# Performance work log

Hardware: AMD Instinct MI355X
Metric: run time of the kernel (lower is better)

The kernel has to match this reference:

```python
import jax, jax.numpy as jnp
import numpy as np


def setup_inputs() -> dict:
    key = jax.random.key(0)
    k_x, k_w1, k_b1, k_w2, k_b2 = jax.random.split(key, 5)
    N, D, H = 4_000_000, 10, 16
    x = jax.random.normal(k_x, (N, D), dtype=jnp.float32)
    # torch.nn.Linear default init: U(-1/sqrt(fan_in), 1/sqrt(fan_in))
    lim1 = 1.0 / np.sqrt(D)
    W1 = jax.random.uniform(k_w1, (H, D), minval=-lim1, maxval=lim1, dtype=jnp.float32)
    b1 = jax.random.uniform(k_b1, (H,), minval=-lim1, maxval=lim1, dtype=jnp.float32)
    lim2 = 1.0 / np.sqrt(H)
    W2 = jax.random.uniform(k_w2, (1, H), minval=-lim2, maxval=lim2, dtype=jnp.float32)
    b2 = jax.random.uniform(k_b2, (1,), minval=-lim2, maxval=lim2, dtype=jnp.float32)
    return {"x": x, "W1": W1, "b1": b1, "W2": W2, "b2": b2}


def reference(x, W1, b1, W2, b2):
    # Gram matrix: (10, 10)
    y = x.T @ x
    # symmetric eigendecomposition; w: eigenvectors (10, 10), ascending eigenvalues
    v, w = jnp.linalg.eigh(y)
    h = jax.nn.relu(w @ W1.T + b1)          # (10, 16)
    o = h @ W2.T + b2                        # (10, 1)
    return 0.5 * (jax.nn.sigmoid(o) + 1.0)
```

## Files before the change

### kernel.cpp

```cpp
#include <hip/hip_runtime.h>
#include <math.h>

#pragma clang fp contract(off)

#define NACC 55
#define KC_DEFAULT 384
#define FOLD_LDS 12288

__device__ __forceinline__ void group_load(const float4* __restrict__ xv,
                                           long g, float4* buf) {
#pragma unroll
  for (int t = 0; t < 20; ++t) buf[t] = xv[g * 20 + t];
}

__device__ __forceinline__ void pair_fma_one(const float4 q0, const float4 q1,
                                             const float4 q2, const float4 q3,
                                             const float4 q4, float* acc) {
  float a[10] = {q0.x, q0.y, q0.z, q0.w, q1.x, q1.y, q1.z, q1.w, q2.x, q2.y};
  float b[10] = {q2.z, q2.w, q3.x, q3.y, q3.z, q3.w, q4.x, q4.y, q4.z, q4.w};
  int e = 0;
#pragma unroll
  for (int i = 0; i < 10; ++i)
#pragma unroll
    for (int j = 0; j <= i; ++j) {
      acc[e] = __builtin_fmaf(a[i], a[j], acc[e]);
      acc[e] = __builtin_fmaf(b[i], b[j], acc[e]);
      ++e;
    }
}

__device__ __forceinline__ void group_fma(const float4* buf, float* acc) {
#pragma unroll
  for (int pp = 0; pp < 4; ++pp)
    pair_fma_one(buf[pp * 5 + 0], buf[pp * 5 + 1], buf[pp * 5 + 2],
                 buf[pp * 5 + 3], buf[pp * 5 + 4], acc);
}

__global__ __launch_bounds__(64, 1) void gram32_kernel(
    const float* __restrict__ x, float* __restrict__ partial,
    int nrows, int kc, int nchunks, int prow) {
  int c = blockIdx.x * 64 + threadIdx.x;
  if (c >= nchunks) return;
  long k0 = (long)c * kc;
  long rem = (long)nrows - k0;
  int klen = rem < kc ? (int)rem : kc;

  float acc[NACC];
#pragma unroll
  for (int e = 0; e < NACC; ++e) acc[e] = 0.0f;

  const float4* __restrict__ xv = (const float4*)(x + k0 * 10);
  int npair = klen >> 1;
  int ngrp = npair >> 2;

  float4 bufA[20], bufB[20];

  int g = 0;
  if (ngrp > 0) group_load(xv, 0, bufA);
  while (g < ngrp) {
    if (g + 1 < ngrp) group_load(xv, g + 1, bufB);
    group_fma(bufA, acc);
    ++g;
    if (g >= ngrp) break;
    if (g + 1 < ngrp) group_load(xv, g + 1, bufA);
    group_fma(bufB, acc);
    ++g;
  }
  for (int p = ngrp * 4; p < npair; ++p) {
    float4 v0 = xv[(long)p * 5 + 0];
    float4 v1 = xv[(long)p * 5 + 1];
    float4 v2 = xv[(long)p * 5 + 2];
    float4 v3 = xv[(long)p * 5 + 3];
    float4 v4 = xv[(long)p * 5 + 4];
    pair_fma_one(v0, v1, v2, v3, v4, acc);
  }
  if (klen & 1) {
    const float* row = x + (k0 + klen - 1) * 10;
    float a[10];
#pragma unroll
    for (int i = 0; i < 10; ++i) a[i] = row[i];
    int e = 0;
#pragma unroll
    for (int i = 0; i < 10; ++i)
#pragma unroll
      for (int j = 0; j <= i; ++j) {
        acc[e] = __builtin_fmaf(a[i], a[j], acc[e]);
        ++e;
      }
  }
#pragma unroll
  for (int e = 0; e < NACC; ++e)
    partial[(long)e * prow + c] = acc[e];
}

__global__ __launch_bounds__(256) void fold32_kernel(
    const float* __restrict__ partial, float* __restrict__ G, int nchunks,
    int prow) {
  __shared__ float buf[FOLD_LDS];
  int e = blockIdx.x;
  const float* p = partial + (long)e * prow;

  if (nchunks <= FOLD_LDS) {
    int n4 = nchunks >> 2;
    const float4* p4 = (const float4*)p;
    float4* b4 = (float4*)buf;
    for (int i = threadIdx.x; i < n4; i += 256) b4[i] = p4[i];
    for (int i = (n4 << 2) + threadIdx.x; i < nchunks; i += 256)
      buf[i] = p[i];
    __syncthreads();
    if (threadIdx.x == 0) {
      float s = buf[0];
      int c = 1;
      for (; c + 16 <= nchunks; c += 16) {
        float v[16];
#pragma unroll
        for (int t = 0; t < 16; ++t) v[t] = buf[c + t];
#pragma unroll
        for (int t = 0; t < 16; ++t) s = s + v[t];
      }
      for (; c < nchunks; ++c) s = s + buf[c];
      G[e] = s;
    }
  } else {
    if (threadIdx.x == 0) {
      float s = p[0];
      for (int c = 1; c < nchunks; ++c) s = s + p[c];
      G[e] = s;
    }
  }
}

__device__ __forceinline__ float rdlane(float v, int l) {
  return __int_as_float(__builtin_amdgcn_readlane(__float_as_int(v), l));
}
__device__ __forceinline__ float s_sign(float a, float b) {
  return copysignf(fabsf(a), b);
}
__device__ __forceinline__ float slapy2(float x, float y) {
  float xa = fabsf(x), ya = fabsf(y);
  float w = fmaxf(xa, ya), z = fminf(xa, ya);
  if (z == 0.0f) return w;
  float t = z / w;
  return w * sqrtf(1.0f + t * t);
}
__device__ __forceinline__ void slartg(float f, float g, float* c, float* s,
                                       float* r) {
  float d = sqrtf(f * f + g * g);
  float cg = fabsf(f) / d;
  float rg = s_sign(d, f);
  float sg = g / rg;
  bool g0 = (g == 0.0f);
  bool f0 = (f == 0.0f);
  *c = g0 ? 1.0f : (f0 ? 0.0f : cg);
  *s = g0 ? 0.0f : (f0 ? s_sign(1.0f, g) : sg);
  *r = g0 ? f : (f0 ? fabsf(g) : rg);
}
__device__ void slaev2(float a, float b, float c, float* rt1, float* rt2,
                       float* cs1, float* sn1) {
  float sm = a + c, df = a - c;
  float adf = fabsf(df);
  float tb = b + b;
  float ab = fabsf(tb);
  float acmx, acmn;
  if (fabsf(a) > fabsf(c)) { acmx = a; acmn = c; } else { acmx = c; acmn = a; }
  float rt;
  if (adf > ab) { float t = ab / adf; rt = adf * sqrtf(1.0f + t * t); }
  else if (adf < ab) { float t = adf / ab; rt = ab * sqrtf(1.0f + t * t); }
  else rt = ab * sqrtf(2.0f);
  int sgn1;
  if (sm < 0.0f) {
    *rt1 = 0.5f * (sm - rt); sgn1 = -1;
    *rt2 = (acmx / *rt1) * acmn - (b / *rt1) * b;
  } else if (sm > 0.0f) {
    *rt1 = 0.5f * (sm + rt); sgn1 = 1;
    *rt2 = (acmx / *rt1) * acmn - (b / *rt1) * b;
  } else {
    *rt1 = 0.5f * rt; *rt2 = -0.5f * rt; sgn1 = 1;
  }
  int sgn2;
  float cs;
  if (df >= 0.0f) { cs = df + rt; sgn2 = 1; } else { cs = df - rt; sgn2 = -1; }
  float acs = fabsf(cs);
  if (acs > ab) {
    float ct = -tb / cs;
    *sn1 = 1.0f / sqrtf(1.0f + ct * ct);
    *cs1 = ct * (*sn1);
  } else {
    if (ab == 0.0f) { *cs1 = 1.0f; *sn1 = 0.0f; }
    else {
      float tn = -cs / tb;
      *cs1 = 1.0f / sqrtf(1.0f + tn * tn);
      *sn1 = tn * (*cs1);
    }
  }
  if (sgn1 == sgn2) { float tn = *cs1; *cs1 = -(*sn1); *sn1 = tn; }
}

#define GETD(i) ((i)==0?d0:(i)==1?d1:(i)==2?d2:(i)==3?d3:(i)==4?d4:(i)==5?d5:(i)==6?d6:(i)==7?d7:(i)==8?d8:d9)
#define PUTD(i,v) do{int _i=(i);float _x=(v);d0=(_i==0)?_x:d0;d1=(_i==1)?_x:d1;d2=(_i==2)?_x:d2;d3=(_i==3)?_x:d3;d4=(_i==4)?_x:d4;d5=(_i==5)?_x:d5;d6=(_i==6)?_x:d6;d7=(_i==7)?_x:d7;d8=(_i==8)?_x:d8;d9=(_i==9)?_x:d9;}while(0)
#define GETZ(i) ((i)==0?z0:(i)==1?z1:(i)==2?z2:(i)==3?z3:(i)==4?z4:(i)==5?z5:(i)==6?z6:(i)==7?z7:(i)==8?z8:z9)
#define PUTZ(i,v) do{int _i=(i);float _x=(v);z0=(_i==0)?_x:z0;z1=(_i==1)?_x:z1;z2=(_i==2)?_x:z2;z3=(_i==3)?_x:z3;z4=(_i==4)?_x:z4;z5=(_i==5)?_x:z5;z6=(_i==6)?_x:z6;z7=(_i==7)?_x:z7;z8=(_i==8)?_x:z8;z9=(_i==9)?_x:z9;}while(0)

__global__ __launch_bounds__(64, 1) void solve_kernel(
    const float* __restrict__ Gp, const float* __restrict__ W1,
    const float* __restrict__ b1, const float* __restrict__ W2,
    const float* __restrict__ b2, float* __restrict__ out) {
  __shared__ float zbuf[10 * 11];
  __shared__ float abuf[10 * 11];
  const int lane = threadIdx.x;
  const int myrow = lane < 10 ? lane : 9;

  float row[10];
#pragma unroll
  for (int c = 0; c < 10; ++c) {
    int rr = myrow >= c ? myrow : c;
    int cc = myrow >= c ? c : myrow;
    row[c] = Gp[rr * (rr + 1) / 2 + cc];
  }

  float dv = 0.0f, ev = 0.0f;
  float tau[9];

#pragma unroll
  for (int i = 0; i < 9; ++i) {
    float v[10];
    {
      float myci = row[i];
#pragma unroll
      for (int k = 0; k < 10; ++k) v[k] = rdlane(myci, k);
    }
    float alpha = v[i + 1];
    float xn2 = 0.0f;
#pragma unroll
    for (int k = i + 2; k < 10; ++k) xn2 = xn2 + v[k] * v[k];
    float xnorm = sqrtf(xn2);
    float taui;
    if (xnorm == 0.0f) {
      taui = 0.0f;
      ev = (lane == i) ? alpha : ev;
    } else {
      float beta = -s_sign(slapy2(alpha, xnorm), alpha);
      taui = (beta - alpha) / beta;
      float sc = 1.0f / (alpha - beta);
#pragma unroll
      for (int k = i + 2; k < 10; ++k) v[k] = v[k] * sc;
      if (lane >= i + 2 && lane < 10) row[i] = row[i] * sc;
      if (lane == i) {
#pragma unroll
        for (int c = i + 2; c < 10; ++c) row[c] = row[c] * sc;
      }
      if (lane == i + 1) row[i] = beta;
      if (lane == i) row[i + 1] = beta;
      ev = (lane == i) ? beta : ev;
    }
    if (taui != 0.0f) {
      v[i + 1] = 1.0f;
      float vme = (lane == i + 1)
                      ? 1.0f
                      : ((lane >= i + 2 && lane < 10) ? row[i] : 0.0f);
      float s = 0.0f;
#pragma unroll
      for (int c2 = i + 1; c2 < 10; ++c2) s = s + row[c2] * v[c2];
      float pvr = taui * s;
      float pva[10];
#pragma unroll
      for (int k = 0; k < 10; ++k) pva[k] = rdlane(pvr, k);
      float dot = 0.0f;
#pragma unroll
      for (int k = i + 1; k < 10; ++k) dot = dot + pva[k] * v[k];
      float alpha2 = -0.5f * taui * dot;
      pvr = pvr + alpha2 * vme;
#pragma unroll
      for (int k = 0; k < 10; ++k) pva[k] = pva[k] + alpha2 * v[k];
      if (lane >= i + 1 && lane < 10) {
#pragma unroll
        for (int c2 = i + 1; c2 < 10; ++c2)
          row[c2] = row[c2] - (vme * pva[c2] + pvr * v[c2]);
      }
    }
    tau[i] = taui;
    {
      float t = rdlane(row[i], i);
      dv = (lane == i) ? t : dv;
    }
  }
  {
    float t = rdlane(row[9], 9);
    dv = (lane == 9) ? t : dv;
  }

  float z0, z1, z2, z3, z4, z5, z6, z7, z8, z9;
  z0 = (lane == 0) ? 1.0f : 0.0f;
  z1 = (lane == 1) ? 1.0f : 0.0f;
  z2 = (lane == 2) ? 1.0f : 0.0f;
  z3 = (lane == 3) ? 1.0f : 0.0f;
  z4 = (lane == 4) ? 1.0f : 0.0f;
  z5 = (lane == 5) ? 1.0f : 0.0f;
  z6 = (lane == 6) ? 1.0f : 0.0f;
  z7 = (lane == 7) ? 1.0f : 0.0f;
  z8 = (lane == 8) ? 1.0f : 0.0f;
  z9 = (lane == 9) ? 1.0f : 0.0f;

  const float eps = 5.9604644775390625e-08f;
  const float eps2 = 3.5527136788005009e-15f;
  const float safmin = 1.1754943508222875e-38f;
  const int nmaxit = 300;
  int jtot = 0;
  int l1 = 0;

  while (l1 < 10) {
    if (l1 > 0) ev = (lane == l1 - 1) ? 0.0f : ev;
    int m = 9;
    {
      float dnx = __shfl(dv, (lane + 1) & 63, 64);
      float te = fabsf(ev);
      bool c1 = (te == 0.0f);
      bool c2 = (te <= (sqrtf(fabsf(dv)) * sqrtf(fabsf(dnx))) * eps);
      bool inr = (lane >= l1) && (lane <= 8);
      unsigned long long bal = __ballot(inr && (c1 || c2));
      if (bal) {
        m = __builtin_ctzll(bal);
        ev = ((lane == m) && !c1) ? 0.0f : ev;
      }
    }
    int l = l1, lsv = l, lend = m, lendsv = lend;
    l1 = m + 1;
    if (lend == l) continue;
    float va = (lane >= l && lane <= lend) ? fabsf(dv) : 0.0f;
    float vb = (lane >= l && lane < lend) ? fabsf(ev) : 0.0f;
    float vm = fmaxf(va, vb);
#pragma unroll
    for (int off = 32; off > 0; off >>= 1)
      vm = fmaxf(vm, __shfl_xor(vm, off, 64));
    if (vm == 0.0f) continue;
    {
      float dle = rdlane(dv, lend);
      float dls = rdlane(dv, l);
      if (fabsf(dle) < fabsf(dls)) { lend = lsv; l = lendsv; }
    }

    if (lend > l) {
      for (;;) {
        int m2 = lend;
        if (l != lend) {
          float dnx2 = __shfl(dv, (lane + 1) & 63, 64);
          float t2 = ev * ev;
          bool cnd = (t2 <= (eps2 * fabsf(dv)) * fabsf(dnx2) + safmin);
          bool ir = (lane >= l) && (lane < lend);
          unsigned long long b2 = __ballot(ir && cnd);
          if (b2) m2 = __builtin_ctzll(b2);
        }
        if (m2 < lend) ev = (lane == m2) ? 0.0f : ev;
        float p = rdlane(dv, l);
        if (m2 == l) {
          ++l;
          if (l <= lend) continue;
          break;
        }
        if (m2 == l + 1) {
          float el = rdlane(ev, l);
          float dl1 = rdlane(dv, l + 1);
          float rt1, rt2, cc2, ss2;
          slaev2(p, el, dl1, &rt1, &rt2, &cc2, &ss2);
          float zl = GETZ(l), zl1 = GETZ(l + 1);
          float t = zl1;
          PUTZ(l + 1, cc2 * t - ss2 * zl);
          PUTZ(l, ss2 * t + cc2 * zl);
          dv = (lane == l) ? rt1 : dv;
          dv = (lane == l + 1) ? rt2 : dv;
          ev = (lane == l) ? 0.0f : ev;
          l += 2;
          if (l <= lend) continue;
          break;
        }
        if (jtot == nmaxit) break;
        ++jtot;
        float el = rdlane(ev, l);
        float dl1 = rdlane(dv, l + 1);
        float dm2 = rdlane(dv, m2);
        float g = (dl1 - p) / (2.0f * el);
        float r2 = slapy2(g, 1.0f);
        g = dm2 - p + (el / (g + s_sign(r2, g)));
        float ss = 1.0f, cc = 1.0f;
        p = 0.0f;
        float carry = GETZ(m2);
#pragma clang loop unroll(disable)
        for (int i2 = m2 - 1; i2 >= l; --i2) {
          float ei2 = rdlane(ev, i2);
          float di2 = rdlane(dv, i2);
          float di21 = rdlane(dv, i2 + 1);
          float zj_ = GETZ(i2);
          float f = ss * ei2;
          float bb = cc * ei2;
          slartg(g, f, &cc, &ss, &r2);
          ev = (lane == i2 + 1 && i2 != m2 - 1) ? r2 : ev;
          g = di21 - p;
          r2 = (di2 - g) * ss + 2.0f * cc * bb;
          p = ss * r2;
          dv = (lane == i2 + 1) ? (g + p) : dv;
          g = cc * r2 - bb;
          {
            float cj = cc, sj = -ss;
            float t_ = carry;
            PUTZ(i2 + 1, cj * t_ - sj * zj_);
            carry = sj * t_ + cj * zj_;
          }
        }
        PUTZ(l, carry);
        {
          float dl0 = rdlane(dv, l);
          dv = (lane == l) ? (dl0 - p) : dv;
        }
        ev = (lane == l) ? g : ev;
      }
    } else {
      for (;;) {
        int m2 = lend;
        if (l != lend) {
          float epv = __shfl(ev, (lane - 1) & 63, 64);
          float dpv = __shfl(dv, (lane - 1) & 63, 64);
          float t2 = epv * epv;
          bool cnd = (t2 <= (eps2 * fabsf(dv)) * fabsf(dpv) + safmin);
          bool ir = (lane >= lend + 1) && (lane <= l);
          unsigned long long b2 = __ballot(ir && cnd);
          if (b2) m2 = 63 - __builtin_clzll(b2);
        }
        if (m2 > lend) ev = (lane == m2 - 1) ? 0.0f : ev;
        float p = rdlane(dv, l);
        if (m2 == l) {
          --l;
          if (l >= lend) continue;
          break;
        }
        if (m2 == l - 1) {
          float dlm = rdlane(dv, l - 1);
          float elm = rdlane(ev, l - 1);
          float rt1, rt2, cc2, ss2;
          slaev2(dlm, elm, p, &rt1, &rt2, &cc2, &ss2);
          float zl = GETZ(l), zlm = GETZ(l - 1);
          float t = zl;
          PUTZ(l, cc2 * t - ss2 * zlm);
          PUTZ(l - 1, ss2 * t + cc2 * zlm);
          dv = (lane == l - 1) ? rt1 : dv;
          dv = (lane == l) ? rt2 : dv;
          ev = (lane == l - 1) ? 0.0f : ev;
          l -= 2;
          if (l >= lend) continue;
          break;
        }
        if (jtot == nmaxit) break;
        ++jtot;
        float elm = rdlane(ev, l - 1);
        float dlm = rdlane(dv, l - 1);
        float dm2 = rdlane(dv, m2);
        float g = (dlm - p) / (2.0f * elm);
        float r2 = slapy2(g, 1.0f);
        g = dm2 - p + (elm / (g + s_sign(r2, g)));
        float ss = 1.0f, cc = 1.0f;
        p = 0.0f;
        float carry = GETZ(m2);
#pragma clang loop unroll(disable)
        for (int i2 = m2; i2 <= l - 1; ++i2) {
          float ei2 = rdlane(ev, i2);
          float di2 = rdlane(dv, i2);
          float di21 = rdlane(dv, i2 + 1);
          float zjp1 = GETZ(i2 + 1);
          float f = ss * ei2;
          float bb = cc * ei2;
          slartg(g, f, &cc, &ss, &r2);
          ev = (lane == i2 - 1 && i2 != m2) ? r2 : ev;
          g = di2 - p;
          r2 = (di21 - g) * ss + 2.0f * cc * bb;
          p = ss * r2;
          dv = (lane == i2) ? (g + p) : dv;
          g = cc * r2 - bb;
          {
            float cj = cc, sj = ss;
            float t_ = zjp1;
            float zj_ = carry;
            PUTZ(i2, sj * t_ + cj * zj_);
            carry = cj * t_ - sj * zj_;
          }
        }
        PUTZ(l, carry);
        {
          float dl0 = rdlane(dv, l);
          dv = (lane == l) ? (dl0 - p) : dv;
        }
        ev = (lane == l - 1) ? g : ev;
      }
    }
  }

  float d0 = rdlane(dv, 0), d1 = rdlane(dv, 1);
  float d2 = rdlane(dv, 2), d3 = rdlane(dv, 3);
  float d4 = rdlane(dv, 4), d5 = rdlane(dv, 5);
  float d6 = rdlane(dv, 6), d7 = rdlane(dv, 7);
  float d8 = rdlane(dv, 8), d9 = rdlane(dv, 9);

#pragma unroll
  for (int ii = 1; ii < 10; ++ii) {
    const int i2 = ii - 1;
    int k2 = i2;
    float pmin = GETD(i2);
#pragma unroll
    for (int j = ii; j < 10; ++j) {
      float dj = GETD(j);
      if (dj < pmin) { k2 = j; pmin = dj; }
    }
    if (k2 != i2) {
      PUTD(k2, GETD(i2));
      PUTD(i2, pmin);
      float ti = GETZ(i2);
      float tk = GETZ(k2);
      PUTZ(i2, tk);
      PUTZ(k2, ti);
    }
  }

  if (lane < 10) {
#pragma unroll
    for (int c = 0; c < 10; ++c) zbuf[lane * 11 + c] = GETZ(c);
#pragma unroll
    for (int c = 0; c < 10; ++c) abuf[lane * 11 + c] = row[c];
  }
  __syncthreads();
  float zc[10];
#pragma unroll
  for (int r = 0; r < 10; ++r)
    zc[r] = (lane < 10) ? zbuf[r * 11 + lane] : 0.0f;

#pragma unroll
  for (int i = 8; i >= 0; --i) {
    float taui = tau[i];
    if (taui != 0.0f) {
      float hv[10];
#pragma unroll
      for (int k = 0; k < 10; ++k) hv[k] = abuf[k * 11 + i];
      float w = zc[i + 1];
#pragma unroll
      for (int k2 = i + 2; k2 < 10; ++k2) w = w + hv[k2] * zc[k2];
      w = w * taui;
      zc[i + 1] = zc[i + 1] - w;
#pragma unroll
      for (int k2 = i + 2; k2 < 10; ++k2) zc[k2] = zc[k2] - hv[k2] * w;
    }
  }

  __syncthreads();
  if (lane < 10) {
#pragma unroll
    for (int r = 0; r < 10; ++r) zbuf[r * 11 + lane] = zc[r];
  }
  __syncthreads();
  float zrow[10];
#pragma unroll
  for (int c = 0; c < 10; ++c)
    zrow[c] = (lane < 10) ? zbuf[lane * 11 + c] : 0.0f;

  if (lane < 10) {
    float o = 0.0f;
#pragma unroll
    for (int j = 0; j < 16; ++j) {
      float acc = 0.0f;
#pragma unroll
      for (int k = 0; k < 10; ++k) acc = acc + zrow[k] * W1[j * 10 + k];
      acc = acc + b1[j];
      float h = fmaxf(acc, 0.0f);
      o = o + h * W2[j];
    }
    o = o + b2[0];
    float sig = 1.0f / (1.0f + expf(-o));
    out[lane] = 0.5f * (sig + 1.0f);
  }
}

extern "C" void kernel_launch(void* const* d_in, const int* in_sizes, int n_in,
                              void* d_out, int out_size, void* d_ws,
                              size_t ws_size, hipStream_t stream) {
  const float* x = (const float*)d_in[0];
  const float* W1 = (const float*)d_in[1];
  const float* b1 = (const float*)d_in[2];
  const float* W2 = (const float*)d_in[3];
  const float* b2 = (const float*)d_in[4];
  float* out = (float*)d_out;

  int nrows = in_sizes[0] / 10;

  int kc = KC_DEFAULT;
  for (;;) {
    long nchunks = ((long)nrows + kc - 1) / kc;
    long prow = (nchunks + 63) & ~63L;
    size_t need = (size_t)NACC * prow * sizeof(float) + 256;
    if (need <= ws_size || kc > nrows) break;
    kc *= 2;
  }
  int nchunks = (int)(((long)nrows + kc - 1) / kc);
  int prow = (int)(((long)nchunks + 63) & ~63L);

  float* partial = (float*)d_ws;
  float* G = partial + (size_t)NACC * prow;

  int grid = (nchunks + 63) / 64;
  gram32_kernel<<<grid, 64, 0, stream>>>(x, partial, nrows, kc, nchunks,
                                         prow);
  fold32_kernel<<<NACC, 256, 0, stream>>>(partial, G, nchunks, prow);
  solve_kernel<<<1, 64, 0, stream>>>(G, W1, b1, W2, b2, out);
}
```

Before: 167.9 us.

## Deepen gram load pipeline to four buffers and use DPP shifts in eigensolver

The Gram accumulation loop now rotates through four register buffers and prefetches three groups ahead instead of one, so more global-load latency is hidden behind the FMAs. The cost is much higher VGPR pressure, which could cause spills at the launch bound of 64 threads. In the tridiagonal QL/QR eigensolver, neighbor shuffles become DPP row shifts. The wave-wide max reduction for the norm is replaced by scalar readlane loops over the 10 active lanes, aiming to cut latency in the serial single-wave phase.

```diff
diff --git a/kernel.cpp b/kernel.cpp
--- a/kernel.cpp
+++ b/kernel.cpp
@@ -53,17 +53,27 @@
   int npair = klen >> 1;
   int ngrp = npair >> 2;
 
-  float4 bufA[20], bufB[20];
-
+  float4 b0[20], b1[20], b2[20], b3[20];
+
+  if (ngrp > 0) group_load(xv, 0, b0);
+  if (ngrp > 1) group_load(xv, 1, b1);
+  if (ngrp > 2) group_load(xv, 2, b2);
   int g = 0;
-  if (ngrp > 0) group_load(xv, 0, bufA);
   while (g < ngrp) {
-    if (g + 1 < ngrp) group_load(xv, g + 1, bufB);
-    group_fma(bufA, acc);
+    if (g + 3 < ngrp) group_load(xv, g + 3, b3);
+    group_fma(b0, acc);
     ++g;
     if (g >= ngrp) break;
-    if (g + 1 < ngrp) group_load(xv, g + 1, bufA);
-    group_fma(bufB, acc);
+    if (g + 3 < ngrp) group_load(xv, g + 3, b0);
+    group_fma(b1, acc);
+    ++g;
+    if (g >= ngrp) break;
+    if (g + 3 < ngrp) group_load(xv, g + 3, b1);
+    group_fma(b2, acc);
+    ++g;
+    if (g >= ngrp) break;
+    if (g + 3 < ngrp) group_load(xv, g + 3, b2);
+    group_fma(b3, acc);
     ++g;
   }
   for (int p = ngrp * 4; p < npair; ++p) {
@@ -132,6 +142,14 @@
 
 __device__ __forceinline__ float rdlane(float v, int l) {
   return __int_as_float(__builtin_amdgcn_readlane(__float_as_int(v), l));
+}
+__device__ __forceinline__ float dpp_next(float v) {
+  return __int_as_float(__builtin_amdgcn_update_dpp(
+      0, __float_as_int(v), 0x101, 0xf, 0xf, true));
+}
+__device__ __forceinline__ float dpp_prev(float v) {
+  return __int_as_float(__builtin_amdgcn_update_dpp(
+      0, __float_as_int(v), 0x111, 0xf, 0xf, true));
 }
 __device__ __forceinline__ float s_sign(float a, float b) {
   return copysignf(fabsf(a), b);
@@ -312,7 +330,7 @@
     if (l1 > 0) ev = (lane == l1 - 1) ? 0.0f : ev;
     int m = 9;
     {
-      float dnx = __shfl(dv, (lane + 1) & 63, 64);
+      float dnx = dpp_next(dv);
       float te = fabsf(ev);
       bool c1 = (te == 0.0f);
       bool c2 = (te <= (sqrtf(fabsf(dv)) * sqrtf(fabsf(dnx))) * eps);
@@ -326,13 +344,18 @@
     int l = l1, lsv = l, lend = m, lendsv = lend;
     l1 = m + 1;
     if (lend == l) continue;
-    float va = (lane >= l && lane <= lend) ? fabsf(dv) : 0.0f;
-    float vb = (lane >= l && lane < lend) ? fabsf(ev) : 0.0f;
-    float vm = fmaxf(va, vb);
-#pragma unroll
-    for (int off = 32; off > 0; off >>= 1)
-      vm = fmaxf(vm, __shfl_xor(vm, off, 64));
-    if (vm == 0.0f) continue;
+    float anorm = 0.0f;
+#pragma unroll
+    for (int k = 0; k <= 9; ++k) {
+      float dk = rdlane(dv, k);
+      anorm = fmaxf(anorm, (k >= l && k <= lend) ? fabsf(dk) : 0.0f);
+    }
+#pragma unroll
+    for (int k = 0; k <= 8; ++k) {
+      float ek = rdlane(ev, k);
+      anorm = fmaxf(anorm, (k >= l && k < lend) ? fabsf(ek) : 0.0f);
+    }
+    if (anorm == 0.0f) continue;
     {
       float dle = rdlane(dv, lend);
       float dls = rdlane(dv, l);
@@ -343,7 +366,7 @@
       for (;;) {
         int m2 = lend;
         if (l != lend) {
-          float dnx2 = __shfl(dv, (lane + 1) & 63, 64);
+          float dnx2 = dpp_next(dv);
           float t2 = ev * ev;
           bool cnd = (t2 <= (eps2 * fabsf(dv)) * fabsf(dnx2) + safmin);
           bool ir = (lane >= l) && (lane < lend);
@@ -417,8 +440,8 @@
       for (;;) {
         int m2 = lend;
         if (l != lend) {
-          float epv = __shfl(ev, (lane - 1) & 63, 64);
-          float dpv = __shfl(dv, (lane - 1) & 63, 64);
+          float epv = dpp_prev(ev);
+          float dpv = dpp_prev(dv);
           float t2 = epv * epv;
           bool cnd = (t2 <= (eps2 * fabsf(dv)) * fabsf(dpv) + safmin);
           bool ir = (lane >= lend + 1) && (lane <= l);
```

Result: slower. 181.5 us (+8.1%).
